# Optimization experiments

Hardware: AMD Instinct MI355X
Metric: run time of the kernel (lower is better)

## Reference

```python
import jax, jax.numpy as jnp
import numpy as np

N_NODES = 50000
N_EDGES = 400000
N_GRAPHS = 512
IN_DIM = 768
HID = 64
BN_EPS = 1e-5


def setup_inputs() -> dict:
    key = jax.random.key(0)
    ks = jax.random.split(key, 12)
    x = jax.random.normal(ks[0], (N_NODES, IN_DIM), dtype=jnp.float32)
    edge_index = jax.random.randint(ks[1], (2, N_EDGES), 0, N_NODES, dtype=jnp.int64)
    batch = jnp.sort(jax.random.randint(ks[2], (N_NODES,), 0, N_GRAPHS, dtype=jnp.int64))

    def lin_init(k, fan_in, fan_out):
        kw, kb = jax.random.split(k)
        bound = 1.0 / np.sqrt(fan_in)
        W = jax.random.uniform(kw, (fan_in, fan_out), minval=-bound, maxval=bound, dtype=jnp.float32)
        b = jax.random.uniform(kb, (fan_out,), minval=-bound, maxval=bound, dtype=jnp.float32)
        return W, b

    w1a, b1a = lin_init(ks[3], IN_DIM, HID)
    w1b, b1b = lin_init(ks[4], HID, HID)
    w2a, b2a = lin_init(ks[5], HID, HID)
    w2b, b2b = lin_init(ks[6], HID, HID)
    wl, bl = lin_init(ks[7], 2 * HID, 2)

    ones = jnp.ones((HID,), jnp.float32)
    zeros = jnp.zeros((HID,), jnp.float32)
    return {
        "x": x, "edge_index": edge_index, "batch": batch,
        "w1a": w1a, "b1a": b1a, "g1": ones, "be1": zeros, "rm1": zeros, "rv1": ones,
        "w1b": w1b, "b1b": b1b,
        "w2a": w2a, "b2a": b2a, "g2": ones, "be2": zeros, "rm2": zeros, "rv2": ones,
        "w2b": w2b, "b2b": b2b,
        "wl": wl, "bl": bl,
    }


def _bn_eval(h, gamma, beta, rm, rv):
    # BatchNorm1d in eval mode: normalize with running stats
    return (h - rm) * (gamma * jax.lax.rsqrt(rv + BN_EPS)) + beta


def _gin_conv(x, src, dst, Wa, ba, gamma, beta, rm, rv, Wb, bb):
    # GINConv eps=0: h = MLP(x + sum_{j in N(i)} x_j); messages x[src] scatter-added to dst
    agg = jax.ops.segment_sum(x[src], dst, num_segments=N_NODES)
    h = x + agg
    h = jnp.dot(h, Wa) + ba
    h = jax.nn.relu(_bn_eval(h, gamma, beta, rm, rv))
    return jnp.dot(h, Wb) + bb


def reference(x, edge_index, batch,
              w1a, b1a, g1, be1, rm1, rv1, w1b, b1b,
              w2a, b2a, g2, be2, rm2, rv2, w2b, b2b,
              wl, bl):
    src, dst = edge_index[0], edge_index[1]
    # eval mode: dropout_edge and F.dropout are identity
    x1 = jax.nn.relu(_gin_conv(x, src, dst, w1a, b1a, g1, be1, rm1, rv1, w1b, b1b))
    x2 = jax.nn.relu(_gin_conv(x1, src, dst, w2a, b2a, g2, be2, rm2, rv2, w2b, b2b))
    x_jk = jnp.concatenate([x1, x2], axis=-1)  # [N, 2*HID]
    x_pool = jax.ops.segment_sum(x_jk, batch, num_segments=N_GRAPHS)  # [G, 2*HID]
    return jnp.dot(x_pool, wl) + bl  # [G, 2]
```

## Files before the change

kernel.cpp:

```cpp
#include <hip/hip_runtime.h>

constexpr int N_NODES  = 50000;
constexpr int N_EDGES  = 400000;
constexpr int N_GRAPHS = 512;
constexpr int IN_DIM   = 768;
constexpr int HID      = 64;
constexpr float BN_EPS = 1e-5f;
constexpr int CAP      = 64;

typedef __attribute__((ext_vector_type(8))) short bf16x8;
typedef __attribute__((ext_vector_type(4))) float f32x4;

__device__ __forceinline__ float bf2f(ushort u) {
  return __uint_as_float((unsigned int)u << 16);
}
__device__ __forceinline__ ushort f2bf(float f) {
  unsigned int u = __float_as_uint(f);
  u = (u + 0x7fff + ((u >> 16) & 1)) >> 16;
  return (ushort)u;
}

constexpr int W1A_E = HID * IN_DIM;
constexpr int WB_E  = HID * HID;
__global__ __launch_bounds__(256) void convert_all(
    const float* __restrict__ w1a, const float* __restrict__ w1b,
    const float* __restrict__ w2a, const float* __restrict__ w2b,
    const float* __restrict__ bl,
    ushort* __restrict__ WT, ushort* __restrict__ WT1b,
    ushort* __restrict__ WT2a, ushort* __restrict__ WT2b,
    float* __restrict__ out, int* __restrict__ cnt) {
  int i = blockIdx.x * 256 + threadIdx.x;
  if (i < W1A_E) {
    int c = i / IN_DIM, k = i - c * IN_DIM;
    WT[i] = f2bf(w1a[(size_t)k * HID + c]);
    return;
  }
  int j = i - W1A_E;
  if (j < 3 * WB_E) {
    int w = j / WB_E, r = j - w * WB_E;
    int c = r / HID, k = r - c * HID;
    const float* W = (w == 0) ? w1b : (w == 1) ? w2a : w2b;
    ushort* D = (w == 0) ? WT1b : (w == 1) ? WT2a : WT2b;
    D[r] = f2bf(W[(size_t)k * HID + c]);
    return;
  }
  int o = j - 3 * WB_E;
  if (o < N_GRAPHS * 2) { out[o] = bl[o & 1]; return; }
  int z = o - N_GRAPHS * 2;
  if (z < N_NODES) cnt[z] = 0;
}

constexpr int GB1 = (N_NODES + 127) / 128;
constexpr int BB  = (N_EDGES + 255) / 256;

__global__ __launch_bounds__(256) void gemm_build(const float* __restrict__ X,
                                                  const ushort* __restrict__ WT,
                                                  ushort* __restrict__ P,
                                                  const int* __restrict__ src,
                                                  const int* __restrict__ dst,
                                                  int* __restrict__ cnt,
                                                  int* __restrict__ bucket) {
  const int tid = threadIdx.x;

  if (blockIdx.x >= GB1) {
    int e = (blockIdx.x - GB1) * 256 + tid;
    if (e < N_EDGES) {
      int s = src[e];
      int d = dst[e];
      int slot = atomicAdd(&cnt[d], 1);
      if (slot < CAP) bucket[d * CAP + slot] = s;
    }
    return;
  }

  __shared__ ushort xs[128][64];
  __shared__ ushort ws[64][64];
  const int row0 = blockIdx.x * 128;
  const int wave = tid >> 6, lane = tid & 63, quad = lane >> 4, l16 = lane & 15;

  const int srow = tid >> 1;
  const int sk   = (tid & 1) * 32;
  int gr = row0 + srow;
  gr = gr < N_NODES ? gr : N_NODES - 1;
  const float* xrow = &X[(size_t)gr * IN_DIM + sk];
  const int wrow = tid >> 2;
  const int wc0  = (tid & 3) * 2;
  const ushort* wrp = &WT[(size_t)wrow * IN_DIM + wc0 * 8];

  f32x4 acc[2][4] = {};

  float4 xv[8];
#pragma unroll
  for (int i = 0; i < 8; i++) xv[i] = *(const float4*)&xrow[i * 4];
  uint4 wv0 = *(const uint4*)&wrp[0];
  uint4 wv1 = *(const uint4*)&wrp[8];

  for (int kt = 0; kt < IN_DIM; kt += 64) {
    ushort xb[32];
#pragma unroll
    for (int i = 0; i < 8; i++) {
      xb[i * 4 + 0] = f2bf(xv[i].x);
      xb[i * 4 + 1] = f2bf(xv[i].y);
      xb[i * 4 + 2] = f2bf(xv[i].z);
      xb[i * 4 + 3] = f2bf(xv[i].w);
    }
#pragma unroll
    for (int j = 0; j < 4; j++)
      *(uint4*)&xs[srow][(((sk >> 3) + j) ^ (srow & 7)) * 8] = *(uint4*)&xb[j * 8];
    *(uint4*)&ws[wrow][((wc0 + 0) ^ (wrow & 7)) * 8] = wv0;
    *(uint4*)&ws[wrow][((wc0 + 1) ^ (wrow & 7)) * 8] = wv1;
    __syncthreads();

    if (kt + 64 < IN_DIM) {
#pragma unroll
      for (int i = 0; i < 8; i++) xv[i] = *(const float4*)&xrow[kt + 64 + i * 4];
      wv0 = *(const uint4*)&wrp[kt + 64];
      wv1 = *(const uint4*)&wrp[kt + 64 + 8];
    }

    const int ar0 = wave * 32 + l16;
    const int ar1 = ar0 + 16;
#pragma unroll
    for (int ks = 0; ks < 2; ks++) {
      bf16x8 a0 = *(const bf16x8*)&xs[ar0][((ks * 4 + quad) ^ (ar0 & 7)) * 8];
      bf16x8 a1 = *(const bf16x8*)&xs[ar1][((ks * 4 + quad) ^ (ar1 & 7)) * 8];
#pragma unroll
      for (int ct = 0; ct < 4; ct++) {
        const int br = ct * 16 + l16;
        bf16x8 b = *(const bf16x8*)&ws[br][((ks * 4 + quad) ^ (br & 7)) * 8];
        acc[0][ct] = __builtin_amdgcn_mfma_f32_16x16x32_bf16(a0, b, acc[0][ct], 0, 0, 0);
        acc[1][ct] = __builtin_amdgcn_mfma_f32_16x16x32_bf16(a1, b, acc[1][ct], 0, 0, 0);
      }
    }
    __syncthreads();
  }

#pragma unroll
  for (int g2 = 0; g2 < 2; g2++)
#pragma unroll
    for (int ct = 0; ct < 4; ct++)
#pragma unroll
      for (int r = 0; r < 4; r++) {
        int row = row0 + wave * 32 + g2 * 16 + quad * 4 + r;
        if (row < N_NODES)
          P[(size_t)row * HID + ct * 16 + l16] = f2bf(acc[g2][ct][r]);
      }
}

template <int CHAIN>
__global__ __launch_bounds__(256) void fused_mlp(
    const int* __restrict__ cnt, const int* __restrict__ bucket,
    const ushort* __restrict__ Pin,
    const float* __restrict__ bin, const float* __restrict__ g,
    const float* __restrict__ be, const float* __restrict__ rm,
    const float* __restrict__ rv,
    const ushort* __restrict__ WT1, const float* __restrict__ b1,
    const ushort* __restrict__ WT2, ushort* __restrict__ OUT2,
    const int* __restrict__ batch, const float* __restrict__ wlh,
    float* __restrict__ out) {
  __shared__ ushort xs[64][64];
  __shared__ ushort ws[64][64];
  __shared__ ushort ws2[CHAIN ? 64 : 1][64];
  __shared__ float sS[64], sT[64];
  __shared__ float gacc[N_GRAPHS * 2];
  __shared__ float wl_s[2 * HID];
  const int tid  = threadIdx.x;
  const int row0 = blockIdx.x * 64;
  const int srow = tid >> 2;
  const int sub  = tid & 3;
  const int qc0  = sub * 2;

#pragma unroll
  for (int i = tid; i < N_GRAPHS * 2; i += 256) gacc[i] = 0.0f;
  if (tid < 2 * HID) wl_s[tid] = wlh[tid];
  if (tid < 64) {
    float s = g[tid] * rsqrtf(rv[tid] + BN_EPS);
    sS[tid] = s;
    sT[tid] = (bin[tid] - rm[tid]) * s + be[tid];
  }
  {
    uint4 w0 = *(const uint4*)&WT1[(size_t)srow * HID + qc0 * 8];
    uint4 w1 = *(const uint4*)&WT1[(size_t)srow * HID + qc0 * 8 + 8];
    *(uint4*)&ws[srow][((qc0 + 0) ^ (srow & 7)) * 8] = w0;
    *(uint4*)&ws[srow][((qc0 + 1) ^ (srow & 7)) * 8] = w1;
    if (CHAIN) {
      uint4 v0 = *(const uint4*)&WT2[(size_t)srow * HID + qc0 * 8];
      uint4 v1 = *(const uint4*)&WT2[(size_t)srow * HID + qc0 * 8 + 8];
      *(uint4*)&ws2[srow][((qc0 + 0) ^ (srow & 7)) * 8] = v0;
      *(uint4*)&ws2[srow][((qc0 + 1) ^ (srow & 7)) * 8] = v1;
    }
  }
  __syncthreads();

  {
    int node = row0 + srow;
    node = node < N_NODES ? node : N_NODES - 1;
    float acc[16];
    {
      ushort b0[16];
      const ushort* base = &Pin[(size_t)node * HID + sub * 16];
      *(uint4*)&b0[0] = *(const uint4*)&base[0];
      *(uint4*)&b0[8] = *(const uint4*)&base[8];
#pragma unroll
      for (int j = 0; j < 16; j++) acc[j] = bf2f(b0[j]);
    }
    int c = cnt[node];
    c = c < CAP ? c : CAP;
    const int* bkt = &bucket[node * CAP];
    int i = 0;
    for (; i + 4 <= c; i += 4) {
      int4 s4 = *(const int4*)&bkt[i];
      ushort r0[16], r1[16], r2[16], r3[16];
      const ushort* p0 = &Pin[(size_t)s4.x * HID + sub * 16];
      const ushort* p1 = &Pin[(size_t)s4.y * HID + sub * 16];
      const ushort* p2 = &Pin[(size_t)s4.z * HID + sub * 16];
      const ushort* p3 = &Pin[(size_t)s4.w * HID + sub * 16];
      *(uint4*)&r0[0] = *(const uint4*)&p0[0]; *(uint4*)&r0[8] = *(const uint4*)&p0[8];
      *(uint4*)&r1[0] = *(const uint4*)&p1[0]; *(uint4*)&r1[8] = *(const uint4*)&p1[8];
      *(uint4*)&r2[0] = *(const uint4*)&p2[0]; *(uint4*)&r2[8] = *(const uint4*)&p2[8];
      *(uint4*)&r3[0] = *(const uint4*)&p3[0]; *(uint4*)&r3[8] = *(const uint4*)&p3[8];
#pragma unroll
      for (int j = 0; j < 16; j++)
        acc[j] += (bf2f(r0[j]) + bf2f(r1[j])) + (bf2f(r2[j]) + bf2f(r3[j]));
    }
    for (; i < c; i++) {
      const ushort* p0 = &Pin[(size_t)bkt[i] * HID + sub * 16];
      ushort r0[16];
      *(uint4*)&r0[0] = *(const uint4*)&p0[0]; *(uint4*)&r0[8] = *(const uint4*)&p0[8];
#pragma unroll
      for (int j = 0; j < 16; j++) acc[j] += bf2f(r0[j]);
    }
    ushort hb[16];
#pragma unroll
    for (int j = 0; j < 16; j++) {
      int col = sub * 16 + j;
      float v = fmaxf(fmaf(acc[j], sS[col], sT[col]), 0.0f);
      hb[j] = f2bf(v);
    }
    *(uint4*)&xs[srow][((qc0 + 0) ^ (srow & 7)) * 8] = *(uint4*)&hb[0];
    *(uint4*)&xs[srow][((qc0 + 1) ^ (srow & 7)) * 8] = *(uint4*)&hb[8];
  }
  __syncthreads();

  const int wave = tid >> 6, lane = tid & 63, quad = lane >> 4, l16 = lane & 15;
  const int ar = wave * 16 + l16, axor = ar & 7;

  f32x4 acc1[4] = {};
#pragma unroll
  for (int ks = 0; ks < 2; ks++) {
    bf16x8 a = *(const bf16x8*)&xs[ar][((ks * 4 + quad) ^ axor) * 8];
#pragma unroll
    for (int ct = 0; ct < 4; ct++) {
      const int br = ct * 16 + l16;
      bf16x8 b = *(const bf16x8*)&ws[br][((ks * 4 + quad) ^ (br & 7)) * 8];
      acc1[ct] = __builtin_amdgcn_mfma_f32_16x16x32_bf16(a, b, acc1[ct], 0, 0, 0);
    }
  }

  if (CHAIN) __syncthreads();

  float v[4][4];
#pragma unroll
  for (int ct = 0; ct < 4; ct++) {
    const float bo = b1[ct * 16 + l16];
#pragma unroll
    for (int r = 0; r < 4; r++) v[ct][r] = fmaxf(acc1[ct][r] + bo, 0.0f);
  }

  {
    float p0[4] = {}, p1[4] = {};
#pragma unroll
    for (int ct = 0; ct < 4; ct++) {
      const int col = ct * 16 + l16;
      const float w0 = wl_s[col * 2 + 0], w1 = wl_s[col * 2 + 1];
#pragma unroll
      for (int r = 0; r < 4; r++) {
        p0[r] = fmaf(v[ct][r], w0, p0[r]);
        p1[r] = fmaf(v[ct][r], w1, p1[r]);
      }
    }
#pragma unroll
    for (int m = 1; m < 16; m <<= 1) {
#pragma unroll
      for (int r = 0; r < 4; r++) {
        p0[r] += __shfl_xor(p0[r], m);
        p1[r] += __shfl_xor(p1[r], m);
      }
    }
    if (l16 == 0) {
#pragma unroll
      for (int r = 0; r < 4; r++) {
        int node = row0 + wave * 16 + quad * 4 + r;
        if (node < N_NODES) {
          int gi = batch[node];
          atomicAdd(&gacc[gi * 2 + 0], p0[r]);
          atomicAdd(&gacc[gi * 2 + 1], p1[r]);
        }
      }
    }
  }

  if (CHAIN) {
#pragma unroll
    for (int ct = 0; ct < 4; ct++) {
      const int col = ct * 16 + l16;
#pragma unroll
      for (int r = 0; r < 4; r++) {
        int lrow = wave * 16 + quad * 4 + r;
        xs[lrow][(((col >> 3) ^ (lrow & 7)) * 8) + (col & 7)] = f2bf(v[ct][r]);
      }
    }
    __syncthreads();

    f32x4 acc2[4] = {};
#pragma unroll
    for (int ks = 0; ks < 2; ks++) {
      bf16x8 a = *(const bf16x8*)&xs[ar][((ks * 4 + quad) ^ axor) * 8];
#pragma unroll
      for (int ct = 0; ct < 4; ct++) {
        const int br = ct * 16 + l16;
        bf16x8 b = *(const bf16x8*)&ws2[br][((ks * 4 + quad) ^ (br & 7)) * 8];
        acc2[ct] = __builtin_amdgcn_mfma_f32_16x16x32_bf16(a, b, acc2[ct], 0, 0, 0);
      }
    }
#pragma unroll
    for (int ct = 0; ct < 4; ct++) {
      const int col = ct * 16 + l16;
#pragma unroll
      for (int r = 0; r < 4; r++) {
        int grow = row0 + wave * 16 + quad * 4 + r;
        if (grow < N_NODES) OUT2[(size_t)grow * HID + col] = f2bf(acc2[ct][r]);
      }
    }
  }

  __syncthreads();
#pragma unroll
  for (int i = tid; i < N_GRAPHS * 2; i += 256) {
    float vv = gacc[i];
    if (vv != 0.0f) atomicAdd(&out[i], vv);
  }
}

extern "C" void kernel_launch(void* const* d_in, const int* in_sizes, int n_in,
                              void* d_out, int out_size, void* d_ws, size_t ws_size,
                              hipStream_t stream) {
  const float* x   = (const float*)d_in[0];
  const int*   ei  = (const int*)d_in[1];
  const int*   bat = (const int*)d_in[2];
  const float* w1a = (const float*)d_in[3];
  const float* b1a = (const float*)d_in[4];
  const float* g1  = (const float*)d_in[5];
  const float* be1 = (const float*)d_in[6];
  const float* rm1 = (const float*)d_in[7];
  const float* rv1 = (const float*)d_in[8];
  const float* w1b = (const float*)d_in[9];
  const float* b1b = (const float*)d_in[10];
  const float* w2a = (const float*)d_in[11];
  const float* b2a = (const float*)d_in[12];
  const float* g2  = (const float*)d_in[13];
  const float* be2 = (const float*)d_in[14];
  const float* rm2 = (const float*)d_in[15];
  const float* rv2 = (const float*)d_in[16];
  const float* w2b = (const float*)d_in[17];
  const float* b2b = (const float*)d_in[18];
  const float* wl  = (const float*)d_in[19];
  const float* bl  = (const float*)d_in[20];
  float* out = (float*)d_out;

  const int* src = ei;
  const int* dst = ei + N_EDGES;

  const size_t FB = (size_t)N_NODES * HID;
  ushort* P1   = (ushort*)d_ws;
  ushort* P2   = P1 + FB;
  ushort* WT   = P2 + FB;
  ushort* WT1b = WT + (size_t)W1A_E;
  ushort* WT2a = WT1b + WB_E;
  ushort* WT2b = WT2a + WB_E;
  int* cnt     = (int*)(WT2b + WB_E);
  int* bucket  = cnt + N_NODES;

  const int GBF = (N_NODES + 63) / 64;
  const int CB  = (W1A_E + 3 * WB_E + N_GRAPHS * 2 + N_NODES + 255) / 256;

  convert_all<<<CB, 256, 0, stream>>>(w1a, w1b, w2a, w2b, bl,
                                      WT, WT1b, WT2a, WT2b, out, cnt);
  gemm_build<<<GB1 + BB, 256, 0, stream>>>(x, WT, P1, src, dst, cnt, bucket);
  fused_mlp<1><<<GBF, 256, 0, stream>>>(cnt, bucket, P1, b1a, g1, be1, rm1, rv1,
                                        WT1b, b1b, WT2a, P2, bat, wl, out);
  fused_mlp<0><<<GBF, 256, 0, stream>>>(cnt, bucket, P2, b2a, g2, be2, rm2, rv2,
                                        WT2b, b2b, nullptr, nullptr, bat,
                                        wl + 2 * HID, out);
}
```

Measured before the change: 308.4 us.

## Use hardware bf16 packing, pre-scaled bucket indices, prefetched gathers and sorted-batch pooling range

Replaces the software round-to-nearest bf16 conversion with the packed v_cvt_pk_bf16_f32 instruction and unpacks bf16 pairs directly from 32-bit words. Bucket entries now store src<<6 so gather addresses skip a multiply. Neighbor-index loads are software-prefetched one group ahead, and the node's own row and count are issued before the first barrier. Pooling now caches batch ids in shared memory and only clears and flushes the graph range this tile covers, which relies on batch being sorted. The GEMM moves its barrier after the next-tile global loads. Together these cut ALU work, shared-memory clearing and global atomics.

```diff
diff --git a/kernel.cpp b/kernel.cpp
--- a/kernel.cpp
+++ b/kernel.cpp
@@ -10,14 +10,23 @@
 
 typedef __attribute__((ext_vector_type(8))) short bf16x8;
 typedef __attribute__((ext_vector_type(4))) float f32x4;
+typedef __attribute__((ext_vector_type(2))) float f32x2;
+
+__device__ __forceinline__ unsigned int f2bf2(float lo, float hi) {
+  unsigned int r;
+  asm("v_cvt_pk_bf16_f32 %0, %1, %2" : "=v"(r) : "v"(lo), "v"(hi));
+  return r;
+}
+__device__ __forceinline__ ushort f2bf1(float f) { return (ushort)f2bf2(f, f); }
 
 __device__ __forceinline__ float bf2f(ushort u) {
   return __uint_as_float((unsigned int)u << 16);
 }
-__device__ __forceinline__ ushort f2bf(float f) {
-  unsigned int u = __float_as_uint(f);
-  u = (u + 0x7fff + ((u >> 16) & 1)) >> 16;
-  return (ushort)u;
+__device__ __forceinline__ f32x2 unpk(unsigned int u) {
+  f32x2 v;
+  v.x = __uint_as_float(u << 16);
+  v.y = __uint_as_float(u & 0xffff0000u);
+  return v;
 }
 
 constexpr int W1A_E = HID * IN_DIM;
@@ -32,7 +41,7 @@
   int i = blockIdx.x * 256 + threadIdx.x;
   if (i < W1A_E) {
     int c = i / IN_DIM, k = i - c * IN_DIM;
-    WT[i] = f2bf(w1a[(size_t)k * HID + c]);
+    WT[i] = f2bf1(w1a[(size_t)k * HID + c]);
     return;
   }
   int j = i - W1A_E;
@@ -41,7 +50,7 @@
     int c = r / HID, k = r - c * HID;
     const float* W = (w == 0) ? w1b : (w == 1) ? w2a : w2b;
     ushort* D = (w == 0) ? WT1b : (w == 1) ? WT2a : WT2b;
-    D[r] = f2bf(W[(size_t)k * HID + c]);
+    D[r] = f2bf1(W[(size_t)k * HID + c]);
     return;
   }
   int o = j - 3 * WB_E;
@@ -68,7 +77,7 @@
       int s = src[e];
       int d = dst[e];
       int slot = atomicAdd(&cnt[d], 1);
-      if (slot < CAP) bucket[d * CAP + slot] = s;
+      if (slot < CAP) bucket[d * CAP + slot] = s << 6;
     }
     return;
   }
@@ -96,20 +105,17 @@
   uint4 wv1 = *(const uint4*)&wrp[8];
 
   for (int kt = 0; kt < IN_DIM; kt += 64) {
-    ushort xb[32];
+    unsigned int xw[16];
 #pragma unroll
     for (int i = 0; i < 8; i++) {
-      xb[i * 4 + 0] = f2bf(xv[i].x);
-      xb[i * 4 + 1] = f2bf(xv[i].y);
-      xb[i * 4 + 2] = f2bf(xv[i].z);
-      xb[i * 4 + 3] = f2bf(xv[i].w);
+      xw[i * 2 + 0] = f2bf2(xv[i].x, xv[i].y);
+      xw[i * 2 + 1] = f2bf2(xv[i].z, xv[i].w);
     }
 #pragma unroll
     for (int j = 0; j < 4; j++)
-      *(uint4*)&xs[srow][(((sk >> 3) + j) ^ (srow & 7)) * 8] = *(uint4*)&xb[j * 8];
+      *(uint4*)&xs[srow][(((sk >> 3) + j) ^ (srow & 7)) * 8] = *(const uint4*)&xw[j * 4];
     *(uint4*)&ws[wrow][((wc0 + 0) ^ (wrow & 7)) * 8] = wv0;
     *(uint4*)&ws[wrow][((wc0 + 1) ^ (wrow & 7)) * 8] = wv1;
-    __syncthreads();
 
     if (kt + 64 < IN_DIM) {
 #pragma unroll
@@ -117,6 +123,7 @@
       wv0 = *(const uint4*)&wrp[kt + 64];
       wv1 = *(const uint4*)&wrp[kt + 64 + 8];
     }
+    __syncthreads();
 
     const int ar0 = wave * 32 + l16;
     const int ar1 = ar0 + 16;
@@ -143,7 +150,7 @@
       for (int r = 0; r < 4; r++) {
         int row = row0 + wave * 32 + g2 * 16 + quad * 4 + r;
         if (row < N_NODES)
-          P[(size_t)row * HID + ct * 16 + l16] = f2bf(acc[g2][ct][r]);
+          P[(size_t)row * HID + ct * 16 + l16] = f2bf1(acc[g2][ct][r]);
       }
 }
 
@@ -164,20 +171,34 @@
   __shared__ float sS[64], sT[64];
   __shared__ float gacc[N_GRAPHS * 2];
   __shared__ float wl_s[2 * HID];
+  __shared__ int   sbatch[64];
   const int tid  = threadIdx.x;
   const int row0 = blockIdx.x * 64;
   const int srow = tid >> 2;
   const int sub  = tid & 3;
   const int qc0  = sub * 2;
-
-#pragma unroll
-  for (int i = tid; i < N_GRAPHS * 2; i += 256) gacc[i] = 0.0f;
-  if (tid < 2 * HID) wl_s[tid] = wlh[tid];
+  const int sub16 = sub * 16;
+
+  int node = row0 + srow;
+  node = node < N_NODES ? node : N_NODES - 1;
+  const int c_raw = cnt[node];
+  const int* bkt = &bucket[node * CAP];
+  const int4 pre = *(const int4*)bkt;
+  unsigned int sw[8];
+  {
+    const ushort* sp = &Pin[node * HID + sub16];
+    *(uint4*)&sw[0] = *(const uint4*)&sp[0];
+    *(uint4*)&sw[4] = *(const uint4*)&sp[8];
+  }
+
   if (tid < 64) {
+    int nb = row0 + tid;
+    sbatch[tid] = batch[nb < N_NODES ? nb : N_NODES - 1];
     float s = g[tid] * rsqrtf(rv[tid] + BN_EPS);
     sS[tid] = s;
     sT[tid] = (bin[tid] - rm[tid]) * s + be[tid];
   }
+  if (tid < 2 * HID) wl_s[tid] = wlh[tid];
   {
     uint4 w0 = *(const uint4*)&WT1[(size_t)srow * HID + qc0 * 8];
     uint4 w1 = *(const uint4*)&WT1[(size_t)srow * HID + qc0 * 8 + 8];
@@ -193,53 +214,52 @@
   __syncthreads();
 
   {
-    int node = row0 + srow;
-    node = node < N_NODES ? node : N_NODES - 1;
-    float acc[16];
-    {
-      ushort b0[16];
-      const ushort* base = &Pin[(size_t)node * HID + sub * 16];
-      *(uint4*)&b0[0] = *(const uint4*)&base[0];
-      *(uint4*)&b0[8] = *(const uint4*)&base[8];
-#pragma unroll
-      for (int j = 0; j < 16; j++) acc[j] = bf2f(b0[j]);
-    }
-    int c = cnt[node];
-    c = c < CAP ? c : CAP;
-    const int* bkt = &bucket[node * CAP];
+    f32x2 acc2[8];
+#pragma unroll
+    for (int j = 0; j < 8; j++) acc2[j] = unpk(sw[j]);
+
+    int c = c_raw < CAP ? c_raw : CAP;
     int i = 0;
-    for (; i + 4 <= c; i += 4) {
-      int4 s4 = *(const int4*)&bkt[i];
-      ushort r0[16], r1[16], r2[16], r3[16];
-      const ushort* p0 = &Pin[(size_t)s4.x * HID + sub * 16];
-      const ushort* p1 = &Pin[(size_t)s4.y * HID + sub * 16];
-      const ushort* p2 = &Pin[(size_t)s4.z * HID + sub * 16];
-      const ushort* p3 = &Pin[(size_t)s4.w * HID + sub * 16];
-      *(uint4*)&r0[0] = *(const uint4*)&p0[0]; *(uint4*)&r0[8] = *(const uint4*)&p0[8];
-      *(uint4*)&r1[0] = *(const uint4*)&p1[0]; *(uint4*)&r1[8] = *(const uint4*)&p1[8];
-      *(uint4*)&r2[0] = *(const uint4*)&p2[0]; *(uint4*)&r2[8] = *(const uint4*)&p2[8];
-      *(uint4*)&r3[0] = *(const uint4*)&p3[0]; *(uint4*)&r3[8] = *(const uint4*)&p3[8];
-#pragma unroll
-      for (int j = 0; j < 16; j++)
-        acc[j] += (bf2f(r0[j]) + bf2f(r1[j])) + (bf2f(r2[j]) + bf2f(r3[j]));
+    if (c >= 4) {
+      int4 s4 = pre;
+      for (; i + 4 <= c; i += 4) {
+        const int4 cur = s4;
+        if (i + 8 <= c) s4 = *(const int4*)&bkt[i + 4];
+        unsigned int w0[8], w1[8], w2[8], w3[8];
+        const ushort* p0 = &Pin[cur.x + sub16];
+        const ushort* p1 = &Pin[cur.y + sub16];
+        const ushort* p2 = &Pin[cur.z + sub16];
+        const ushort* p3 = &Pin[cur.w + sub16];
+        *(uint4*)&w0[0] = *(const uint4*)&p0[0]; *(uint4*)&w0[4] = *(const uint4*)&p0[8];
+        *(uint4*)&w1[0] = *(const uint4*)&p1[0]; *(uint4*)&w1[4] = *(const uint4*)&p1[8];
+        *(uint4*)&w2[0] = *(const uint4*)&p2[0]; *(uint4*)&w2[4] = *(const uint4*)&p2[8];
+        *(uint4*)&w3[0] = *(const uint4*)&p3[0]; *(uint4*)&w3[4] = *(const uint4*)&p3[8];
+#pragma unroll
+        for (int j = 0; j < 8; j++)
+          acc2[j] += (unpk(w0[j]) + unpk(w1[j])) + (unpk(w2[j]) + unpk(w3[j]));
+      }
     }
     for (; i < c; i++) {
-      const ushort* p0 = &Pin[(size_t)bkt[i] * HID + sub * 16];
-      ushort r0[16];
-      *(uint4*)&r0[0] = *(const uint4*)&p0[0]; *(uint4*)&r0[8] = *(const uint4*)&p0[8];
-#pragma unroll
-      for (int j = 0; j < 16; j++) acc[j] += bf2f(r0[j]);
-    }
-    ushort hb[16];
-#pragma unroll
-    for (int j = 0; j < 16; j++) {
-      int col = sub * 16 + j;
-      float v = fmaxf(fmaf(acc[j], sS[col], sT[col]), 0.0f);
-      hb[j] = f2bf(v);
-    }
-    *(uint4*)&xs[srow][((qc0 + 0) ^ (srow & 7)) * 8] = *(uint4*)&hb[0];
-    *(uint4*)&xs[srow][((qc0 + 1) ^ (srow & 7)) * 8] = *(uint4*)&hb[8];
-  }
+      const ushort* p0 = &Pin[bkt[i] + sub16];
+      unsigned int w0[8];
+      *(uint4*)&w0[0] = *(const uint4*)&p0[0]; *(uint4*)&w0[4] = *(const uint4*)&p0[8];
+#pragma unroll
+      for (int j = 0; j < 8; j++) acc2[j] += unpk(w0[j]);
+    }
+
+    unsigned int hw[8];
+#pragma unroll
+    for (int j = 0; j < 8; j++) {
+      const int col = sub16 + j * 2;
+      float x0 = fmaxf(fmaf(acc2[j].x, sS[col],     sT[col]),     0.0f);
+      float x1 = fmaxf(fmaf(acc2[j].y, sS[col + 1], sT[col + 1]), 0.0f);
+      hw[j] = f2bf2(x0, x1);
+    }
+    *(uint4*)&xs[srow][((qc0 + 0) ^ (srow & 7)) * 8] = *(const uint4*)&hw[0];
+    *(uint4*)&xs[srow][((qc0 + 1) ^ (srow & 7)) * 8] = *(const uint4*)&hw[4];
+  }
+  const int g0 = sbatch[0], g1 = sbatch[63];
+  for (int z = g0 * 2 + tid; z <= g1 * 2 + 1; z += 256) gacc[z] = 0.0f;
   __syncthreads();
 
   const int wave = tid >> 6, lane = tid & 63, quad = lane >> 4, l16 = lane & 15;
@@ -290,9 +310,9 @@
     if (l16 == 0) {
 #pragma unroll
       for (int r = 0; r < 4; r++) {
-        int node = row0 + wave * 16 + quad * 4 + r;
-        if (node < N_NODES) {
-          int gi = batch[node];
+        int lrow = wave * 16 + quad * 4 + r;
+        if (row0 + lrow < N_NODES) {
+          int gi = sbatch[lrow];
           atomicAdd(&gacc[gi * 2 + 0], p0[r]);
           atomicAdd(&gacc[gi * 2 + 1], p1[r]);
         }
@@ -307,12 +327,12 @@
 #pragma unroll
       for (int r = 0; r < 4; r++) {
         int lrow = wave * 16 + quad * 4 + r;
-        xs[lrow][(((col >> 3) ^ (lrow & 7)) * 8) + (col & 7)] = f2bf(v[ct][r]);
+        xs[lrow][(((col >> 3) ^ (lrow & 7)) * 8) + (col & 7)] = f2bf1(v[ct][r]);
       }
     }
     __syncthreads();
 
-    f32x4 acc2[4] = {};
+    f32x4 accB[4] = {};
 #pragma unroll
     for (int ks = 0; ks < 2; ks++) {
       bf16x8 a = *(const bf16x8*)&xs[ar][((ks * 4 + quad) ^ axor) * 8];
@@ -320,7 +340,7 @@
       for (int ct = 0; ct < 4; ct++) {
         const int br = ct * 16 + l16;
         bf16x8 b = *(const bf16x8*)&ws2[br][((ks * 4 + quad) ^ (br & 7)) * 8];
-        acc2[ct] = __builtin_amdgcn_mfma_f32_16x16x32_bf16(a, b, acc2[ct], 0, 0, 0);
+        accB[ct] = __builtin_amdgcn_mfma_f32_16x16x32_bf16(a, b, accB[ct], 0, 0, 0);
       }
     }
 #pragma unroll
@@ -329,16 +349,15 @@
 #pragma unroll
       for (int r = 0; r < 4; r++) {
         int grow = row0 + wave * 16 + quad * 4 + r;
-        if (grow < N_NODES) OUT2[(size_t)grow * HID + col] = f2bf(acc2[ct][r]);
+        if (grow < N_NODES) OUT2[(size_t)grow * HID + col] = f2bf1(accB[ct][r]);
       }
     }
   }
 
   __syncthreads();
-#pragma unroll
-  for (int i = tid; i < N_GRAPHS * 2; i += 256) {
-    float vv = gacc[i];
-    if (vv != 0.0f) atomicAdd(&out[i], vv);
+  for (int z = g0 * 2 + tid; z <= g1 * 2 + 1; z += 256) {
+    float vv = gacc[z];
+    if (vv != 0.0f) atomicAdd(&out[z], vv);
   }
 }
 
```

Result: no change. 304.7 us (-1.2%).
